# Kernel optimization log

Measured on AMD Instinct MI355X. Metric: run time of the kernel, lower is better.

## Reference

```python
import jax, jax.numpy as jnp
import numpy as np


def setup_inputs() -> dict:
    key = jax.random.key(0)
    k1, = jax.random.split(key, 1)
    B, L, D = 128, 1024, 768
    hidden_states = jax.random.normal(k1, (B, L, D), dtype=jnp.float32)
    attention_mask = jnp.zeros((B, 1, 1, L), dtype=jnp.float32)
    return {"hidden_states": hidden_states, "attention_mask": attention_mask, "K": 512}


def reference(hidden_states, attention_mask, K):
    B, L, D = hidden_states.shape
    # r tokens to merge, protected class token (ToMe: r = min(r, (t - protected)//2))
    r = max(0, L - K)
    r = min(r, (L - 1) // 2)

    # --- bipartite soft matching (indices computed under no_grad in torch) ---
    metric = hidden_states / jnp.linalg.norm(hidden_states, axis=-1, keepdims=True)
    a = metric[:, ::2, :]   # [B, t1, D] even tokens (src side)
    b = metric[:, 1::2, :]  # [B, t2, D] odd tokens (dst side)
    scores = jnp.einsum('bid,bjd->bij', a, b)  # [B, t1, t2]
    scores = scores.at[:, 0, :].set(-jnp.inf)  # protect class token (row 0 of src)
    node_max = jnp.max(scores, axis=-1)        # [B, t1]
    node_idx = jnp.argmax(scores, axis=-1)     # [B, t1] best dst per src
    order = jnp.argsort(-node_max, axis=-1)    # descending similarity
    src_idx = order[:, :r]                     # [B, r] tokens to merge away
    unm_idx = jnp.sort(order[:, r:], axis=-1)  # [B, t1-r] kept src tokens (sorted: class_token=True)
    dst_idx = jnp.take_along_axis(node_idx, src_idx, axis=-1)  # [B, r]

    # --- merge(x, mode='mean') with include_self=True ---
    src = hidden_states[:, ::2, :]   # [B, t1, D]
    dst = hidden_states[:, 1::2, :]  # [B, t2, D]
    t2 = dst.shape[1]
    unm = jnp.take_along_axis(src, unm_idx[..., None], axis=1)     # [B, t1-r, D]
    src_g = jnp.take_along_axis(src, src_idx[..., None], axis=1)   # [B, r, D]
    bidx = jnp.arange(B)[:, None]
    dst_sum = dst.at[bidx, dst_idx].add(src_g)                     # self + merged srcs
    counts = jnp.ones((B, t2), dtype=hidden_states.dtype).at[bidx, dst_idx].add(1.0)
    dst_mean = dst_sum / counts[..., None]

    preserved_tokens = jnp.concatenate([unm, dst_mean], axis=1)    # [B, t1-r+t2, D]
    final_attention_mask = jnp.zeros((B, 1, 1, preserved_tokens.shape[1]),
                                     dtype=hidden_states.dtype)
    return preserved_tokens, final_attention_mask
```

## Files before the change

kernel.cpp:

```cpp
#include <hip/hip_runtime.h>
#include <hip/hip_bf16.h>

#define B_ 128
#define L_ 1024
#define T_ 512
#define D_ 768
#define CH_ 96
#define DT_ 513
#define TAU_C 1e-3f
#define PBUF_ 1024

#define KS_B_CSTR 8208
#define KS_B_BYTES (4 * KS_B_CSTR)
#define KS_A_CSTR 2064
#define KS_A_BYTES (4 * KS_A_CSTR)
#define KS_BYTES (KS_B_BYTES + KS_A_BYTES)
#define SMEM_BYTES (3 * KS_BYTES)

typedef __attribute__((ext_vector_type(8))) short bf16x8;
typedef __attribute__((ext_vector_type(4))) float f32x4;

typedef const __attribute__((address_space(1))) unsigned int* gas1_t;
typedef __attribute__((address_space(3))) unsigned int* gas3_t;

__device__ __forceinline__ unsigned short f2bf_rne(float x){
    unsigned u = __float_as_uint(x);
    unsigned r = (u + 0x7FFFu + ((u >> 16) & 1u)) >> 16;
    return (unsigned short)r;
}

__global__ __launch_bounds__(256) void pack_k(const float* __restrict__ hs,
                                              unsigned short* __restrict__ Apk,
                                              unsigned short* __restrict__ Bpk,
                                              double* __restrict__ nsq,
                                              int* __restrict__ paircnt){
    __shared__ __align__(16) unsigned short LhS[CH_ * 16 * 8];
    if (blockIdx.x == 0 && threadIdx.x == 0) *paircnt = 0;
    int b = blockIdx.x >> 6, g = blockIdx.x & 63;
    int wv = threadIdx.x >> 6, lane = threadIdx.x & 63;

    #pragma unroll
    for (int rr = 0; rr < 4; ++rr){
        int jj = wv * 4 + rr;
        long seq = (long)b * L_ + g * 16 + jj;
        const float4* src = (const float4*)(hs + seq * D_);
        float4 f0 = src[lane], f1 = src[lane + 64], f2 = src[lane + 128];
        double s = 0.0;
        s += (double)f0.x*f0.x + (double)f0.y*f0.y + (double)f0.z*f0.z + (double)f0.w*f0.w;
        s += (double)f1.x*f1.x + (double)f1.y*f1.y + (double)f1.z*f1.z + (double)f1.w*f1.w;
        s += (double)f2.x*f2.x + (double)f2.y*f2.y + (double)f2.z*f2.z + (double)f2.w*f2.w;
        #pragma unroll
        for (int off = 32; off; off >>= 1) s += __shfl_xor(s, off);
        if (lane == 0 && (jj & 1)) nsq[seq] = s;
        float rn = (float)(1.0 / sqrt(s));
        float4 fv[3] = {f0, f1, f2};
        #pragma unroll
        for (int t = 0; t < 3; ++t){
            int e0 = t * 256 + lane * 4;
            int c = e0 >> 3, ei = e0 & 7;
            float vv[4] = {fv[t].x, fv[t].y, fv[t].z, fv[t].w};
            short4 hv;
            #pragma unroll
            for (int e = 0; e < 4; ++e)
                ((short*)&hv)[e] = (short)f2bf_rne(vv[e] * rn);
            int o = c * 128 + ((jj ^ (c & 7)) << 3) + ei;
            *(short4*)(LhS + o) = hv;
        }
    }
    __syncthreads();
    #pragma unroll
    for (int it = 0; it < 6; ++it){
        int linear = it * 256 + threadIdx.x;
        int c = linear >> 4, jj = linear & 15;
        int o = c * 128 + ((jj ^ (c & 7)) << 3);
        int tok = g * 8 + (jj >> 1);
        long go = ((long)(b * CH_ + c) * T_ + tok) * 8;
        if (jj & 1) *(bf16x8*)(Bpk + go) = *(const bf16x8*)(LhS + o);
        else        *(bf16x8*)(Apk + go) = *(const bf16x8*)(LhS + o);
    }
}

__global__ __launch_bounds__(512, 2) void coarse_k(const unsigned short* __restrict__ Apk,
                                                   const unsigned short* __restrict__ Bpk,
                                                   int* __restrict__ node_idx,
                                                   unsigned long long* __restrict__ rowkey,
                                                   int* __restrict__ paircnt,
                                                   int2* __restrict__ pairs){
    __shared__ __align__(16) char SMEM[SMEM_BYTES];

    int bid = blockIdx.x;
    int xcd = bid & 7, q = bid >> 3;
    int it = q & 3, bhi = q >> 2;
    int b = xcd + 8 * bhi;

    int tid = threadIdx.x;
    int w = tid >> 6, lane = tid & 63, l15 = lane & 15, l4 = lane >> 4;
    int wr = w >> 2, wc = w & 3;

    long pkbase = (long)b * CH_ * T_;

    #define STAGE(s_, slot_) do {                                                          \
        char* dst_ = SMEM + (slot_) * KS_BYTES;                                            \
        _Pragma("unroll")                                                                  \
        for (int n_ = 0; n_ < 4; ++n_){                                                    \
            const unsigned short* sp_ = Bpk + (pkbase + (long)((s_)*4 + n_) * T_ + w * 64 + lane) * 8; \
            __builtin_amdgcn_global_load_lds((gas1_t)sp_, (gas3_t)(dst_ + n_ * KS_B_CSTR + w * 1024), 16, 0, 0); \
        }                                                                                  \
        {                                                                                  \
            const unsigned short* sp_ = Apk + (pkbase + (long)((s_)*4 + (w >> 1)) * T_ + it * 128 + (w & 1) * 64 + lane) * 8; \
            __builtin_amdgcn_global_load_lds((gas1_t)sp_, (gas3_t)(dst_ + KS_B_BYTES + (w >> 1) * KS_A_CSTR + (w & 1) * 1024), 16, 0, 0); \
        }                                                                                  \
    } while (0)

    STAGE(0, 0); STAGE(1, 1);

    f32x4 acc[4][8];
    #pragma unroll
    for (int i = 0; i < 4; ++i)
        #pragma unroll
        for (int j = 0; j < 8; ++j) acc[i][j] = (f32x4){0.f, 0.f, 0.f, 0.f};

    __syncthreads();

    #pragma unroll 3
    for (int s = 0; s < 24; ++s){
        if (s < 22) STAGE(s + 2, (s + 2) % 3);
        const char* slot = SMEM + (s % 3) * KS_BYTES;
        bf16x8 ah[4], bh[8];
        #pragma unroll
        for (int ib = 0; ib < 4; ++ib)
            ah[ib] = *(const bf16x8*)(slot + KS_B_BYTES + l4 * KS_A_CSTR + (wr * 64 + ib * 16 + l15) * 16);
        #pragma unroll
        for (int jb = 0; jb < 8; ++jb)
            bh[jb] = *(const bf16x8*)(slot + l4 * KS_B_CSTR + (wc * 128 + jb * 16 + l15) * 16);
        __builtin_amdgcn_s_setprio(1);
        #pragma unroll
        for (int jb = 0; jb < 8; ++jb)
            #pragma unroll
            for (int ib = 0; ib < 4; ++ib)
                acc[ib][jb] = __builtin_amdgcn_mfma_f32_16x16x32_bf16(ah[ib], bh[jb], acc[ib][jb], 0, 0, 0);
        __builtin_amdgcn_s_setprio(0);
        if (s < 22)      asm volatile("s_waitcnt vmcnt(5)" ::: "memory");
        else             asm volatile("s_waitcnt vmcnt(0)" ::: "memory");
        __builtin_amdgcn_s_barrier();
        asm volatile("" ::: "memory");
    }
    #undef STAGE

    float* pm1s = (float*)SMEM;
    int*   pjs  = (int*)(SMEM + 2048);
    float* m1f  = (float*)(SMEM + 4096);
    int*   cnd  = (int*)(SMEM + 4608);
    int2*  pbuf = (int2*)(SMEM + 5120);
    int*   pcnt_s  = (int*)(SMEM + 13312);
    int*   pbase_s = (int*)(SMEM + 13316);

    #pragma unroll
    for (int ib = 0; ib < 4; ++ib)
        #pragma unroll
        for (int rr = 0; rr < 4; ++rr){
            float m1 = -1e30f; int j1 = 0;
            #pragma unroll
            for (int jb = 0; jb < 8; ++jb){
                float v = acc[ib][jb][rr];
                int col = wc * 128 + jb * 16 + l15;
                if (v > m1){ m1 = v; j1 = col; }
            }
            #pragma unroll
            for (int m = 1; m < 16; m <<= 1){
                float o1 = __shfl_xor(m1, m);
                int   oj = __shfl_xor(j1, m);
                if (o1 > m1 || (o1 == m1 && oj < j1)){ m1 = o1; j1 = oj; }
            }
            if (l15 == 0){
                int row = wr * 64 + ib * 16 + l4 * 4 + rr;
                pm1s[row * 4 + wc] = m1; pjs[row * 4 + wc] = j1;
            }
        }
    __syncthreads();
    int grow0 = b * T_ + it * 128;
    if (tid < 128){
        float M1 = -1e30f; int J1 = 0;
        #pragma unroll
        for (int c2 = 0; c2 < 4; ++c2){
            float a1 = pm1s[tid * 4 + c2]; int aj = pjs[tid * 4 + c2];
            if (a1 > M1 || (a1 == M1 && aj < J1)){ M1 = a1; J1 = aj; }
        }
        node_idx[grow0 + tid] = J1;
        m1f[tid] = M1;
        cnd[tid] = 0;
        rowkey[grow0 + tid] = 0ULL;
        if (tid == 0) *pcnt_s = 0;
    }
    __syncthreads();
    #pragma unroll
    for (int ib = 0; ib < 4; ++ib)
        #pragma unroll
        for (int rr = 0; rr < 4; ++rr){
            int row = wr * 64 + ib * 16 + l4 * 4 + rr;
            float thr_ = m1f[row] - TAU_C;
            int hits = 0;
            #pragma unroll
            for (int jb = 0; jb < 8; ++jb) hits += (acc[ib][jb][rr] > thr_) ? 1 : 0;
            #pragma unroll
            for (int m = 1; m < 16; m <<= 1) hits += __shfl_xor(hits, m);
            if (l15 == 0 && hits) atomicAdd(&cnd[row], hits);
        }
    __syncthreads();
    #pragma unroll
    for (int ib = 0; ib < 4; ++ib)
        #pragma unroll
        for (int rr = 0; rr < 4; ++rr){
            int row = wr * 64 + ib * 16 + l4 * 4 + rr;
            if (cnd[row] < 2) continue;
            if (it == 0 && row == 0) continue;
            float thr_ = m1f[row] - TAU_C;
            #pragma unroll
            for (int jb = 0; jb < 8; ++jb)
                if (acc[ib][jb][rr] > thr_){
                    int idx = atomicAdd(pcnt_s, 1);
                    int2 pr = make_int2(grow0 + row, wc * 128 + jb * 16 + l15);
                    if (idx < PBUF_) pbuf[idx] = pr;
                    else { int p = atomicAdd(paircnt, 1); pairs[p] = pr; }
                }
        }
    __syncthreads();
    if (tid == 0) *pbase_s = atomicAdd(paircnt, min(*pcnt_s, PBUF_));
    __syncthreads();
    int n = min(*pcnt_s, PBUF_);
    for (int k2 = tid; k2 < n; k2 += 512) pairs[*pbase_s + k2] = pbuf[k2];
}

__global__ __launch_bounds__(256) void refine_k(const float* __restrict__ hs,
                                                const double* __restrict__ nsq,
                                                const int* __restrict__ paircnt,
                                                const int2* __restrict__ pairs,
                                                unsigned long long* __restrict__ rowkey){
    int n = *paircnt;
    int w = threadIdx.x >> 6, lane = threadIdx.x & 63;
    for (int p = blockIdx.x * 4 + w; p < n; p += gridDim.x * 4){
        int2 pr = pairs[p];
        int grow = pr.x, j = pr.y;
        int b = grow >> 9, i = grow & 511;
        const float* ar = hs + ((long)b * L_ + 2 * i) * D_;
        const float* br = hs + ((long)b * L_ + 2 * j + 1) * D_;
        double s = 0.0;
        #pragma unroll
        for (int dd = 0; dd < 12; ++dd){
            int d = dd * 64 + lane;
            s += (double)ar[d] * (double)br[d];
        }
        #pragma unroll
        for (int off = 32; off; off >>= 1) s += __shfl_xor(s, off);
        if (lane == 0){
            double sc = s / sqrt(nsq[(long)b * L_ + 2 * j + 1]);
            unsigned long long bits = (unsigned long long)__double_as_longlong(sc);
            unsigned long long key = (bits >> 63) ? ~bits : (bits | 0x8000000000000000ULL);
            key = (key & ~0xFFFFULL) | (unsigned long long)(511 - j);
            atomicMax(&rowkey[grow], key);
        }
    }
}

__global__ __launch_bounds__(512) void csr_k(const int* __restrict__ node_idx,
                                             const unsigned long long* __restrict__ rowkey,
                                             int* __restrict__ goff,
                                             int* __restrict__ glist){
    __shared__ int sidx[512];
    __shared__ int off[513];
    __shared__ int tmp[512];
    __shared__ int cnt[512];
    int b = blockIdx.x, t = threadIdx.x;
    unsigned long long rk = rowkey[b * T_ + t];
    sidx[t] = rk ? (511 - (int)(rk & 0xFFFFULL)) : node_idx[b * T_ + t];
    cnt[t] = 0;
    __syncthreads();
    if (t >= 1) atomicAdd(&cnt[sidx[t]], 1);
    __syncthreads();
    tmp[t] = cnt[t];
    __syncthreads();
    for (int s = 1; s < 512; s <<= 1){
        int v = (t >= s) ? tmp[t - s] : 0;
        __syncthreads();
        tmp[t] += v;
        __syncthreads();
    }
    if (t == 0) off[0] = 0;
    off[t + 1] = tmp[t];
    __syncthreads();
    if (t >= 1){
        int j = sidx[t], r = 0;
        for (int i2 = 1; i2 < t; ++i2) r += (sidx[i2] == j);
        glist[b * T_ + off[j] + r] = t;
    }
    goff[b * 513 + t] = off[t];
    if (t == 0) goff[b * 513 + 512] = off[512];
}

__global__ __launch_bounds__(192) void merge_k(const float* __restrict__ hs,
                                               const int* __restrict__ goff,
                                               const int* __restrict__ glist,
                                               float* __restrict__ out){
    int bid = blockIdx.x;
    int b = bid / DT_, jj = bid - b * DT_;
    long obase4 = ((long)b * DT_ + jj) * (D_ / 4);
    float4* out4 = (float4*)out;
    if (threadIdx.x == 0) out[(long)B_ * DT_ * D_ + b * DT_ + jj] = 0.0f;
    int d = threadIdx.x;
    if (jj == 0){
        const float4* src = (const float4*)(hs + (long)b * L_ * D_);
        out4[obase4 + d] = src[d];
        return;
    }
    int j = jj - 1;
    int o0 = goff[b * 513 + j], o1 = goff[b * 513 + j + 1];
    const float4* dst = (const float4*)(hs + ((long)b * L_ + 2 * j + 1) * D_);
    float4 a = dst[d];
    for (int s = o0; s < o1; ++s){
        int i = glist[b * T_ + s];
        const float4* srow = (const float4*)(hs + ((long)b * L_ + 2 * i) * D_);
        float4 v = srow[d];
        a.x += v.x; a.y += v.y; a.z += v.z; a.w += v.w;
    }
    float rc = 1.0f / (float)(o1 - o0 + 1);
    a.x *= rc; a.y *= rc; a.z *= rc; a.w *= rc;
    out4[obase4 + d] = a;
}

extern "C" void kernel_launch(void* const* d_in, const int* in_sizes, int n_in,
                              void* d_out, int out_size, void* d_ws, size_t ws_size,
                              hipStream_t stream){
    const float* hs = (const float*)d_in[0];
    float* out = (float*)d_out;
    char* ws = (char*)d_ws;

    const long PSZ = (long)B_ * CH_ * T_ * 8;
    unsigned short* Apk = (unsigned short*)ws;
    unsigned short* Bpk = Apk + PSZ;
    double* nsq      = (double*)(ws + 201326592);
    int*    node_idx = (int*)   (ws + 202375168);
    unsigned long long* rowkey = (unsigned long long*)(ws + 202637312);
    int*    paircnt  = (int*)   (ws + 203161600);
    int*    goff     = (int*)   (ws + 203161856);
    int*    glist    = (int*)   (ws + 203425024);
    int2*   pairs    = (int2*)  (ws + 203687168);

    pack_k  <<<B_ * 64, 256, 0, stream>>>(hs, Apk, Bpk, nsq, paircnt);
    coarse_k<<<512, 512, 0, stream>>>(Apk, Bpk, node_idx, rowkey, paircnt, pairs);
    refine_k<<<512, 256, 0, stream>>>(hs, nsq, paircnt, pairs, rowkey);
    csr_k   <<<B_, 512, 0, stream>>>(node_idx, rowkey, goff, glist);
    merge_k <<<B_ * DT_, 192, 0, stream>>>(hs, goff, glist, out);
}
```

Measured before the change: 328.5 us.

## Load A fragments directly to registers and deepen B LDS pipeline to four stages

The A operand of the coarse similarity GEMM is now loaded from global memory straight into double-buffered registers instead of being staged through LDS. The LDS space this frees holds a four-slot B ring with three stages in flight, and the vmcnt waits are retuned to match. This is meant to cut LDS traffic and hide global latency better, at the cost of more VGPRs and relying on hand-counted vmcnt values being correct.

```diff
diff --git a/kernel.cpp b/kernel.cpp
--- a/kernel.cpp
+++ b/kernel.cpp
@@ -12,10 +12,7 @@
 
 #define KS_B_CSTR 8208
 #define KS_B_BYTES (4 * KS_B_CSTR)
-#define KS_A_CSTR 2064
-#define KS_A_BYTES (4 * KS_A_CSTR)
-#define KS_BYTES (KS_B_BYTES + KS_A_BYTES)
-#define SMEM_BYTES (3 * KS_BYTES)
+#define SMEM_BYTES (4 * KS_B_BYTES)
 
 typedef __attribute__((ext_vector_type(8))) short bf16x8;
 typedef __attribute__((ext_vector_type(4))) float f32x4;
@@ -98,21 +95,23 @@
     int wr = w >> 2, wc = w & 3;
 
     long pkbase = (long)b * CH_ * T_;
-
-    #define STAGE(s_, slot_) do {                                                          \
-        char* dst_ = SMEM + (slot_) * KS_BYTES;                                            \
+    const unsigned short* pA = Apk + (pkbase + (long)l4 * T_ + it * 128 + wr * 64 + l15) * 8;
+    const long AKS = (long)4 * T_ * 8;
+
+    #define STAGE_B(s_, slot_) do {                                                        \
+        char* dst_ = SMEM + (slot_) * KS_B_BYTES;                                          \
         _Pragma("unroll")                                                                  \
         for (int n_ = 0; n_ < 4; ++n_){                                                    \
             const unsigned short* sp_ = Bpk + (pkbase + (long)((s_)*4 + n_) * T_ + w * 64 + lane) * 8; \
             __builtin_amdgcn_global_load_lds((gas1_t)sp_, (gas3_t)(dst_ + n_ * KS_B_CSTR + w * 1024), 16, 0, 0); \
         }                                                                                  \
-        {                                                                                  \
-            const unsigned short* sp_ = Apk + (pkbase + (long)((s_)*4 + (w >> 1)) * T_ + it * 128 + (w & 1) * 64 + lane) * 8; \
-            __builtin_amdgcn_global_load_lds((gas1_t)sp_, (gas3_t)(dst_ + KS_B_BYTES + (w >> 1) * KS_A_CSTR + (w & 1) * 1024), 16, 0, 0); \
-        }                                                                                  \
     } while (0)
 
-    STAGE(0, 0); STAGE(1, 1);
+    #define LOAD_A(s_, ar_) do {                                                           \
+        _Pragma("unroll")                                                                  \
+        for (int ib_ = 0; ib_ < 4; ++ib_)                                                  \
+            ar_[ib_] = *(const bf16x8*)(pA + (long)(s_) * AKS + ib_ * 16 * 8);             \
+    } while (0)
 
     f32x4 acc[4][8];
     #pragma unroll
@@ -120,32 +119,46 @@
         #pragma unroll
         for (int j = 0; j < 8; ++j) acc[i][j] = (f32x4){0.f, 0.f, 0.f, 0.f};
 
-    __syncthreads();
-
-    #pragma unroll 3
+    bf16x8 arA[4], arB[4];
+    STAGE_B(0, 0); STAGE_B(1, 1); STAGE_B(2, 2);
+    LOAD_A(0, arA); LOAD_A(1, arB);
+    __syncthreads();
+
+    #pragma unroll 4
     for (int s = 0; s < 24; ++s){
-        if (s < 22) STAGE(s + 2, (s + 2) % 3);
-        const char* slot = SMEM + (s % 3) * KS_BYTES;
-        bf16x8 ah[4], bh[8];
-        #pragma unroll
-        for (int ib = 0; ib < 4; ++ib)
-            ah[ib] = *(const bf16x8*)(slot + KS_B_BYTES + l4 * KS_A_CSTR + (wr * 64 + ib * 16 + l15) * 16);
+        const char* slot = SMEM + (s & 3) * KS_B_BYTES;
+        bf16x8 bh[8];
         #pragma unroll
         for (int jb = 0; jb < 8; ++jb)
             bh[jb] = *(const bf16x8*)(slot + l4 * KS_B_CSTR + (wc * 128 + jb * 16 + l15) * 16);
         __builtin_amdgcn_s_setprio(1);
-        #pragma unroll
-        for (int jb = 0; jb < 8; ++jb)
-            #pragma unroll
-            for (int ib = 0; ib < 4; ++ib)
-                acc[ib][jb] = __builtin_amdgcn_mfma_f32_16x16x32_bf16(ah[ib], bh[jb], acc[ib][jb], 0, 0, 0);
+        if (s & 1){
+            #pragma unroll
+            for (int jb = 0; jb < 8; ++jb)
+                #pragma unroll
+                for (int ib = 0; ib < 4; ++ib)
+                    acc[ib][jb] = __builtin_amdgcn_mfma_f32_16x16x32_bf16(arB[ib], bh[jb], acc[ib][jb], 0, 0, 0);
+        } else {
+            #pragma unroll
+            for (int jb = 0; jb < 8; ++jb)
+                #pragma unroll
+                for (int ib = 0; ib < 4; ++ib)
+                    acc[ib][jb] = __builtin_amdgcn_mfma_f32_16x16x32_bf16(arA[ib], bh[jb], acc[ib][jb], 0, 0, 0);
+        }
         __builtin_amdgcn_s_setprio(0);
-        if (s < 22)      asm volatile("s_waitcnt vmcnt(5)" ::: "memory");
-        else             asm volatile("s_waitcnt vmcnt(0)" ::: "memory");
+        if (s < 22){
+            if (s & 1) LOAD_A(s + 2, arB);
+            else       LOAD_A(s + 2, arA);
+        }
+        if (s < 21) STAGE_B(s + 3, (s + 3) & 3);
+        if (s <= 20)      asm volatile("s_waitcnt vmcnt(12)" ::: "memory");
+        else if (s == 21) asm volatile("s_waitcnt vmcnt(8)"  ::: "memory");
+        else              asm volatile("s_waitcnt vmcnt(0)"  ::: "memory");
         __builtin_amdgcn_s_barrier();
         asm volatile("" ::: "memory");
     }
-    #undef STAGE
+    #undef STAGE_B
+    #undef LOAD_A
 
     float* pm1s = (float*)SMEM;
     int*   pjs  = (int*)(SMEM + 2048);
```

Measured after the change: 348.3 us. +6.0%, slower.
